# Optimization experiments

Hardware: AMD Instinct MI355X
Metric: run time of the kernel (lower is better)

Reference implementation:

```python
import jax, jax.numpy as jnp
import numpy as np

B, S, D = 4, 2048, 1024
H = 8
HD = D // H            # 128 head dim
FF = 4096 // H         # 512 per-head expert hidden
E = 8                  # num experts
K = 2                  # top-k
MU, GAMMA = 0.7, 1.0
LN_EPS = 1e-5


def setup_inputs() -> dict:
    key = jax.random.key(0)
    ks = jax.random.split(key, 12)
    sc = lambda *shape: 1.0 / np.sqrt(shape[0])
    return {
        "x": jax.random.normal(ks[0], (B, S, D), jnp.float32),
        "momentum": jnp.zeros((B * S * H, HD), jnp.float32),
        # split proj (input_dim -> input_dim)
        "split_W": jax.random.normal(ks[1], (D, D), jnp.float32) * sc(D),
        "split_b": jnp.zeros((D,), jnp.float32),
        # gate (head_dim -> num_experts)
        "gate_W": jax.random.normal(ks[2], (HD, E), jnp.float32) * sc(HD),
        "gate_b": jnp.zeros((E,), jnp.float32),
        # stacked experts: Linear(HD->FF) ReLU Linear(FF->HD)
        "W1": jax.random.normal(ks[3], (E, HD, FF), jnp.float32) * sc(HD),
        "b1": jnp.zeros((E, FF), jnp.float32),
        "W2": jax.random.normal(ks[4], (E, FF, HD), jnp.float32) * sc(FF),
        "b2": jnp.zeros((E, HD), jnp.float32),
        # layernorm over head_dim
        "ln_g": jnp.ones((HD,), jnp.float32),
        "ln_b": jnp.zeros((HD,), jnp.float32),
        # merge proj
        "merge_W": jax.random.normal(ks[5], (D, D), jnp.float32) * sc(D),
        "merge_b": jnp.zeros((D,), jnp.float32),
    }


def _topk_gate(t, gate_W, gate_b):
    # t: [T, HD] -> dense gate weights [T, E] with only top-K nonzero
    logits = t @ gate_W + gate_b                       # [T, E]
    topv, topi = jax.lax.top_k(logits, K)              # [T, K]
    gates_k = jax.nn.softmax(topv, axis=-1)            # softmax over kept experts
    onehot = jax.nn.one_hot(topi, E, dtype=t.dtype)    # [T, K, E]
    return jnp.einsum("tk,tke->te", gates_k, onehot)   # scatter back


def reference(x, momentum, split_W, split_b, gate_W, gate_b,
              W1, b1, W2, b2, ln_g, ln_b, merge_W, merge_b):
    # split: [B,S,D] -> [B*S*H, HD]
    x_hat = x @ split_W + split_b
    t = x_hat.reshape(B * S * H, HD)

    gates = _topk_gate(t, gate_W, gate_b)              # [T, E]

    # all-experts dense compute (matches the source's per-expert loop)
    h = jax.nn.relu(jnp.einsum("td,edf->etf", t, W1) + b1[:, None, :])  # [E,T,FF]
    eo = jnp.einsum("etf,efd->etd", h, W2) + b2[:, None, :]             # [E,T,HD]
    expert_outputs = jnp.einsum("te,etd->td", gates, eo)                # [T,HD]

    new_momentum = -expert_outputs + MU * momentum
    out = t + GAMMA * new_momentum

    # layernorm over head_dim
    mean = out.mean(-1, keepdims=True)
    var = out.var(-1, keepdims=True)
    out = (out - mean) * jax.lax.rsqrt(var + LN_EPS) * ln_g + ln_b

    # merge: [T,HD] -> [B,S,D] -> linear
    o = out.reshape(B, S, D)
    final = o @ merge_W + merge_b
    return final, new_momentum
```

## Files before the change

kernel.cpp:

```cpp
#include <hip/hip_runtime.h>

#define NBATCH 4
#define NS 2048
#define ND 1024
#define NH 8
#define HD 128
#define NFF 512
#define NE 8
#define NT 65536
#define NBS 8192
#define MU_F 0.7f
#define LN_EPS_F 1e-5f
#define EPS_GATE 1e-4f

typedef __attribute__((ext_vector_type(4))) float f32x4;
typedef __attribute__((ext_vector_type(2))) double f64x2;
typedef __attribute__((ext_vector_type(8))) _Float16 f16x8;
typedef __attribute__((ext_vector_type(4))) _Float16 f16x4;
typedef __attribute__((ext_vector_type(2))) _Float16 f16x2;

__device__ __forceinline__ void gload_lds16(const void* g, void* l) {
  __builtin_amdgcn_global_load_lds(
      (const __attribute__((address_space(1))) unsigned int*)g,
      (__attribute__((address_space(3))) unsigned int*)l, 16, 0, 0);
}

__global__ void tr_cvt_all_kernel(const float* __restrict__ split_W, const float* __restrict__ merge_W,
                                  const float* __restrict__ W1, const float* __restrict__ W2,
                                  _Float16* __restrict__ sWt, _Float16* __restrict__ mWt,
                                  _Float16* __restrict__ W1t, _Float16* __restrict__ W2t) {
  __shared__ float tile[32][33];
  int id = blockIdx.x;
  const float* in; _Float16* out; int R, C, bx, by, b;
  if (id < 1024)      { in = split_W; out = sWt; R = ND;  C = ND;  bx = id & 31; by = id >> 5; b = 0; }
  else if (id < 2048) { id -= 1024; in = merge_W; out = mWt; R = ND;  C = ND;  bx = id & 31; by = id >> 5; b = 0; }
  else if (id < 2560) { id -= 2048; in = W1; out = W1t; R = HD;  C = NFF; bx = id & 15; by = (id >> 4) & 3; b = id >> 6; }
  else                { id -= 2560; in = W2; out = W2t; R = NFF; C = HD;  bx = id & 3;  by = (id >> 2) & 15; b = id >> 6; }
  const float* inp = in + (size_t)b * R * C;
  _Float16* outp = out + (size_t)b * R * C;
  int c = bx * 32 + threadIdx.x;
  int r0 = by * 32;
  #pragma unroll
  for (int i = 0; i < 4; i++) {
    int r = r0 + threadIdx.y + i * 8;
    tile[threadIdx.y + i * 8][threadIdx.x] = inp[(size_t)r * C + c];
  }
  __syncthreads();
  int rr = r0 + threadIdx.x;
  #pragma unroll
  for (int i = 0; i < 4; i++) {
    int cc = bx * 32 + threadIdx.y + i * 8;
    outp[(size_t)cc * R + rr] = (_Float16)tile[threadIdx.x][threadIdx.y + i * 8];
  }
}

__global__ void build_G_kernel(const float* __restrict__ split_W, const float* __restrict__ split_b,
                               const float* __restrict__ gate_W, const float* __restrict__ gate_b,
                               double* __restrict__ G, float* __restrict__ Gq,
                               double* __restrict__ gbias, int* __restrict__ cnt) {
  int idx = blockIdx.x * 256 + threadIdx.x;
  if (blockIdx.x == 0 && threadIdx.x < 256) { cnt[threadIdx.x] = 0; cnt[threadIdx.x + 256] = 0; }
  int d = idx >> 6, o = idx & 63, h = o >> 3, e = o & 7;
  double acc = 0.0;
  const float* r0 = split_W + (size_t)d * ND + h * 128;
  #pragma unroll 4
  for (int j = 0; j < 128; j++)
    acc += (double)r0[j] * (double)gate_W[j * 8 + e];
  G[((size_t)(d >> 1) * 64 + o) * 2 + (d & 1)] = acc;
  Gq[((size_t)(d >> 2) * 64 + o) * 4 + (d & 3)] = (float)acc;
  if (idx < 64) {
    double bacc = 0.0;
    for (int j = 0; j < 128; j++)
      bacc += (double)split_b[h * 128 + j] * (double)gate_W[j * 8 + e];
    gbias[idx] = bacc + (double)gate_b[e];
  }
}

__global__ __launch_bounds__(256) void gate_kernel(const float* __restrict__ x,
    const float* __restrict__ Gq, const f64x2* __restrict__ Gx2, const double* __restrict__ gbias,
    _Float16* __restrict__ x_h,
    float* __restrict__ tkw, int* __restrict__ lists, int* __restrict__ cnt) {
  __shared__ float Gsq[16 * 256];
  __shared__ float xsf[16 * 68];
  __shared__ float lg[16 * 64];
  __shared__ int lcnt[8];
  __shared__ int lbase[8];
  int tid = threadIdx.x, lane = tid & 63, w = tid >> 6;
  int bs0 = blockIdx.x * 16;
  float accA[4], accB[4];
  #pragma unroll
  for (int r = 0; r < 4; r++) { accA[r] = 0.f; accB[r] = 0.f; }
  int xrow = tid >> 4, xc4 = tid & 15;
  const float* xr = xsf + (w * 4) * 68;
  if (tid < 8) lcnt[tid] = 0;

  for (int ch = 0; ch < 16; ch++) {
    __syncthreads();
    float4 xv4 = *(const float4*)(x + (size_t)(bs0 + xrow) * ND + ch * 64 + xc4 * 4);
    *(float4*)&xsf[xrow * 68 + xc4 * 4] = xv4;
    f16x4 xh = { (_Float16)xv4.x, (_Float16)xv4.y, (_Float16)xv4.z, (_Float16)xv4.w };
    *(f16x4*)(x_h + (size_t)(bs0 + xrow) * ND + ch * 64 + xc4 * 4) = xh;
    #pragma unroll
    for (int j = 0; j < 4; j++) {
      int n = j * 256 + tid;
      gload_lds16(Gq + (size_t)ch * 4096 + n * 4, Gsq + n * 4);
    }
    __syncthreads();
    #pragma unroll 4
    for (int kq = 0; kq < 16; kq++) {
      float4 g = *(const float4*)&Gsq[kq * 256 + lane * 4];
      #pragma unroll
      for (int r = 0; r < 4; r++) {
        float4 xv = *(const float4*)(xr + r * 68 + kq * 4);
        accA[r] = fmaf(xv.x, g.x, accA[r]);
        accB[r] = fmaf(xv.y, g.y, accB[r]);
        accA[r] = fmaf(xv.z, g.z, accA[r]);
        accB[r] = fmaf(xv.w, g.w, accB[r]);
      }
    }
  }
  float gbf = (float)gbias[lane];
  #pragma unroll
  for (int r = 0; r < 4; r++)
    lg[(w * 4 + r) * 64 + lane] = accA[r] + accB[r] + gbf;
  __syncthreads();

  int i1 = 0, i2 = 0, token = 0, p1 = 0, p2 = 0;
  if (tid < 128) {
    int row = tid >> 3, h = tid & 7;
    const float* L = lg + row * 64 + h * 8;
    float v1 = L[0];
    #pragma unroll
    for (int e2 = 1; e2 < 8; e2++) if (L[e2] > v1) { v1 = L[e2]; i1 = e2; }
    i2 = -1; float v2 = -1e30f;
    #pragma unroll
    for (int e2 = 0; e2 < 8; e2++) if (e2 != i1 && L[e2] > v2) { v2 = L[e2]; i2 = e2; }
    float v3 = -1e30f;
    #pragma unroll
    for (int e2 = 0; e2 < 8; e2++) if (e2 != i1 && e2 != i2 && L[e2] > v3) v3 = L[e2];
    float g1 = 0.f, g2 = 0.f;
    bool amb = !((v1 - v2 >= EPS_GATE) && (v2 - v3 >= EPS_GATE));
    if (!amb) {
      float ex = expf(v2 - v1);
      float den = 1.f + ex;
      g1 = 1.f / den; g2 = ex / den;
    }
    unsigned long long mask = __ballot(amb);
    while (mask) {
      int src = __ffsll((long long)mask) - 1;
      mask &= mask - 1;
      int srow = __shfl(row, src, 64);
      int sh   = __shfl(h, src, 64);
      double part[8];
      #pragma unroll
      for (int e2 = 0; e2 < 8; e2++) part[e2] = 0.0;
      const float* xg = x + (size_t)(bs0 + srow) * ND + lane * 16;
      #pragma unroll
      for (int kk = 0; kk < 8; kk++) {
        double x0 = (double)xg[kk * 2], x1 = (double)xg[kk * 2 + 1];
        const f64x2* gp = Gx2 + (size_t)(lane * 8 + kk) * 64 + sh * 8;
        #pragma unroll
        for (int e2 = 0; e2 < 8; e2++) {
          f64x2 g = gp[e2];
          part[e2] += x0 * g.x + x1 * g.y;
        }
      }
      #pragma unroll
      for (int m = 1; m < 64; m <<= 1)
        #pragma unroll
        for (int e2 = 0; e2 < 8; e2++) part[e2] += __shfl_xor(part[e2], m, 64);
      if (lane == src) {
        double L64[8];
        #pragma unroll
        for (int e2 = 0; e2 < 8; e2++) L64[e2] = part[e2] + gbias[sh * 8 + e2];
        i1 = 0; double d1 = L64[0];
        #pragma unroll
        for (int e2 = 1; e2 < 8; e2++) if (L64[e2] > d1) { d1 = L64[e2]; i1 = e2; }
        i2 = -1; double d2 = -1e300;
        #pragma unroll
        for (int e2 = 0; e2 < 8; e2++) if (e2 != i1 && L64[e2] > d2) { d2 = L64[e2]; i2 = e2; }
        float ex = expf((float)(d2 - d1));
        float den = 1.f + ex;
        g1 = 1.f / den; g2 = ex / den;
      }
    }
    token = (bs0 + row) * 8 + h;
    tkw[token * 2]     = g1;
    tkw[token * 2 + 1] = g2;
    p1 = atomicAdd(&lcnt[i1], 1);
    p2 = atomicAdd(&lcnt[i2], 1);
  }
  __syncthreads();
  if (tid < 8) lbase[tid] = atomicAdd(cnt + tid * 64, lcnt[tid]);
  __syncthreads();
  if (tid < 128) {
    lists[(size_t)i1 * NT + lbase[i1] + p1] = token * 2;
    lists[(size_t)i2 * NT + lbase[i2] + p2] = token * 2 + 1;
  }
}

__global__ __launch_bounds__(256) void gemm_f16_kernel(
    const _Float16* __restrict__ A, const _Float16* __restrict__ Bt,
    const float* __restrict__ bias, float* __restrict__ Cf, _Float16* __restrict__ Ch,
    int M, int N, int Kd) {
  __shared__ _Float16 As[128 * 32];
  __shared__ _Float16 Bs[128 * 32];
  int tid = threadIdx.x, lane = tid & 63, w = tid >> 6;
  int wr = w >> 1, wc = w & 1;
  int lid = blockIdx.y * 8 + blockIdx.x;
  int xcd = lid & 7, sub = (lid >> 3) & 7, grp = lid >> 6;
  int m0 = (xcd * 8 + sub) * 128;
  int n0 = grp * 128;
  f32x4 acc[4][4];
  #pragma unroll
  for (int i = 0; i < 4; i++)
    #pragma unroll
    for (int j = 0; j < 4; j++) acc[i][j] = (f32x4){0.f, 0.f, 0.f, 0.f};
  int srow = lane >> 2, scol = (lane & 3) * 8;
  int fr = lane & 15, ko = (lane >> 4) * 8;
  const _Float16* Ag = A + (size_t)(m0 + srow) * Kd + scol;
  const _Float16* Bg = Bt + (size_t)(n0 + srow) * Kd + scol;

  for (int k0 = 0; k0 < Kd; k0 += 32) {
    #pragma unroll
    for (int j = 0; j < 2; j++) {
      int rb = (w * 2 + j) * 16;
      gload_lds16(Ag + (size_t)rb * Kd + k0, As + rb * 32);
      gload_lds16(Bg + (size_t)rb * Kd + k0, Bs + rb * 32);
    }
    __syncthreads();
    f16x8 af[4], bq[4];
    #pragma unroll
    for (int mi = 0; mi < 4; mi++) af[mi] = *(const f16x8*)(As + (wr * 64 + mi * 16 + fr) * 32 + ko);
    #pragma unroll
    for (int ni = 0; ni < 4; ni++) bq[ni] = *(const f16x8*)(Bs + (wc * 64 + ni * 16 + fr) * 32 + ko);
    __syncthreads();
    #pragma unroll
    for (int mi = 0; mi < 4; mi++)
      #pragma unroll
      for (int ni = 0; ni < 4; ni++)
        acc[mi][ni] = __builtin_amdgcn_mfma_f32_16x16x32_f16(af[mi], bq[ni], acc[mi][ni], 0, 0, 0);
  }
  int rbase = m0 + wr * 64 + ((lane >> 4) << 2);
  int cbase = n0 + wc * 64 + (lane & 15);
  #pragma unroll
  for (int mi = 0; mi < 4; mi++)
    #pragma unroll
    for (int ni = 0; ni < 4; ni++) {
      int cc = cbase + ni * 16;
      float bv = bias ? bias[cc] : 0.f;
      #pragma unroll
      for (int r = 0; r < 4; r++) {
        int rr = rbase + mi * 16 + r;
        float v = acc[mi][ni][r] + bv;
        if (Cf) Cf[(size_t)rr * N + cc] = v;
        if (Ch) Ch[(size_t)rr * N + cc] = (_Float16)v;
      }
    }
}

__global__ __launch_bounds__(512, 2) void expert_kernel(
    const _Float16* __restrict__ t_h, const _Float16* __restrict__ W1t, const _Float16* __restrict__ W2t,
    const float* __restrict__ b1, const float* __restrict__ b2,
    const int* __restrict__ cnt, const int* __restrict__ lists, const float* __restrict__ tkw,
    _Float16* __restrict__ slots) {
  int e = blockIdx.x & 7;
  int m0 = (blockIdx.x >> 3) * 128;
  int count = cnt[e * 64];
  if (m0 >= count) return;
  __shared__ _Float16 ring[3][64 * 128];
  __shared__ _Float16 h_s[128 * 64];
  __shared__ float b1s[NFF];
  __shared__ float b2s[HD];
  __shared__ int alist[128];
  __shared__ float aw[128];
  int tid = threadIdx.x, lane = tid & 63, w = tid >> 6;
  int wr = w >> 1, wc = w & 1;
  int fr = lane & 15, g = lane >> 4;

  if (tid < 128) {
    int idx = m0 + tid;
    int a = (idx < count) ? lists[(size_t)e * NT + idx] : -1;
    alist[tid] = a;
    aw[tid] = (a >= 0) ? tkw[a] : 0.f;
  }
  b1s[tid] = b1[e * NFF + tid];
  if (tid < 128) b2s[tid] = b2[e * HD + tid];
  __syncthreads();

  auto stage = [&](int p) {
    if (p >= 16) return;
    int ch = p >> 1;
    _Float16* dst = &ring[p % 3][0];
    if ((p & 1) == 0) {
      #pragma unroll
      for (int j = 0; j < 2; j++) {
        int n = j * 512 + tid;
        int r = n >> 4, gg = n & 15;
        int sg = gg ^ ((r >> 1) & 7);
        gload_lds16(W1t + (size_t)e * (NFF * HD) + (size_t)(ch * 64 + r) * HD + sg * 8, dst + n * 8);
      }
    } else {
      #pragma unroll
      for (int j = 0; j < 2; j++) {
        int n = j * 512 + tid;
        int r = n >> 3, gg = n & 7;
        int sg = gg ^ ((r >> 1) & 7);
        gload_lds16(W2t + (size_t)e * (HD * NFF) + (size_t)r * NFF + ch * 64 + sg * 8, dst + n * 8);
      }
    }
  };

  f16x8 af[2][4];
  #pragma unroll
  for (int mi = 0; mi < 2; mi++) {
    int rloc = wr * 32 + mi * 16 + fr;
    int a = alist[rloc];
    const _Float16* tb = t_h + (size_t)(a >> 1) * HD;
    #pragma unroll
    for (int ks = 0; ks < 4; ks++) {
      f16x8 v = {0, 0, 0, 0, 0, 0, 0, 0};
      if (a >= 0) v = *(const f16x8*)(tb + ks * 32 + g * 8);
      af[mi][ks] = v;
    }
  }
  asm volatile("s_waitcnt vmcnt(0)" ::: "memory");
  stage(0); stage(1);
  asm volatile("s_waitcnt vmcnt(2) lgkmcnt(0)\n\ts_barrier" ::: "memory");

  f32x4 acc2[2][4];
  #pragma unroll
  for (int i = 0; i < 2; i++)
    #pragma unroll
    for (int j = 0; j < 4; j++) acc2[i][j] = (f32x4){0.f, 0.f, 0.f, 0.f};

  #pragma unroll
  for (int p = 0; p < 16; p++) {
    stage(p + 2);
    int ch = p >> 1;
    const char* WB = (const char*)&ring[p % 3][0];
    if ((p & 1) == 0) {
      float b1r[2][4];
      #pragma unroll
      for (int ni = 0; ni < 2; ni++)
        #pragma unroll
        for (int r = 0; r < 4; r++)
          b1r[ni][r] = b1s[ch * 64 + wc * 32 + ni * 16 + g * 4 + r];
      f32x4 acc1[2][2];
      #pragma unroll
      for (int i = 0; i < 2; i++)
        #pragma unroll
        for (int j = 0; j < 2; j++) acc1[i][j] = (f32x4){0.f, 0.f, 0.f, 0.f};
      #pragma unroll
      for (int ks = 0; ks < 4; ks++) {
        f16x8 bq[2];
        #pragma unroll
        for (int ni = 0; ni < 2; ni++) {
          int rw = wc * 32 + ni * 16 + fr;
          int byte = rw * 256 + ((ks * 64 + g * 16) ^ (((rw >> 1) & 7) << 4));
          bq[ni] = *(const f16x8*)(WB + byte);
        }
        #pragma unroll
        for (int mi = 0; mi < 2; mi++)
          #pragma unroll
          for (int ni = 0; ni < 2; ni++)
            acc1[mi][ni] = __builtin_amdgcn_mfma_f32_16x16x32_f16(bq[ni], af[mi][ks], acc1[mi][ni], 0, 0, 0);
      }
      #pragma unroll
      for (int mi = 0; mi < 2; mi++)
        #pragma unroll
        for (int ni = 0; ni < 2; ni++) {
          f16x4 hv;
          #pragma unroll
          for (int r = 0; r < 4; r++)
            hv[r] = (_Float16)fmaxf(acc1[mi][ni][r] + b1r[ni][r], 0.f);
          int tok = wr * 32 + mi * 16 + fr;
          int foff = wc * 64 + ni * 32 + g * 8;
          int byte = tok * 128 + (foff ^ (((tok >> 1) & 7) << 4));
          *(f16x4*)((char*)h_s + byte) = hv;
        }
    } else {
      #pragma unroll
      for (int ks = 0; ks < 2; ks++) {
        f16x8 ah[2], bq[4];
        #pragma unroll
        for (int mi = 0; mi < 2; mi++) {
          int row = wr * 32 + mi * 16 + fr;
          int byte = row * 128 + ((ks * 64 + g * 16) ^ (((row >> 1) & 7) << 4));
          ah[mi] = *(const f16x8*)((const char*)h_s + byte);
        }
        #pragma unroll
        for (int ni = 0; ni < 4; ni++) {
          int rw = wc * 64 + ni * 16 + fr;
          int byte = rw * 128 + ((ks * 64 + g * 16) ^ (((rw >> 1) & 7) << 4));
          bq[ni] = *(const f16x8*)((const char*)&ring[p % 3][0] + byte);
        }
        #pragma unroll
        for (int mi = 0; mi < 2; mi++)
          #pragma unroll
          for (int ni = 0; ni < 4; ni++)
            acc2[mi][ni] = __builtin_amdgcn_mfma_f32_16x16x32_f16(ah[mi], bq[ni], acc2[mi][ni], 0, 0, 0);
      }
    }
    if (p == 14) {
      asm volatile("s_waitcnt vmcnt(0) lgkmcnt(0)\n\ts_barrier" ::: "memory");
    } else if (p < 14) {
      asm volatile("s_waitcnt vmcnt(2) lgkmcnt(0)\n\ts_barrier" ::: "memory");
    }
  }
  #pragma unroll
  for (int mi = 0; mi < 2; mi++)
    #pragma unroll
    for (int ni = 0; ni < 4; ni++) {
      int ncol = wc * 64 + ni * 16 + fr;
      float bv = b2s[ncol];
      #pragma unroll
      for (int r = 0; r < 4; r++) {
        int m = wr * 32 + mi * 16 + g * 4 + r;
        int a = alist[m];
        if (a >= 0)
          slots[(size_t)a * HD + ncol] = (_Float16)(aw[m] * (acc2[mi][ni][r] + bv));
      }
    }
}

__global__ __launch_bounds__(256) void combine_ln_kernel(
    const _Float16* __restrict__ slots, const float* __restrict__ momentum,
    const _Float16* __restrict__ t_h, const float* __restrict__ ln_g, const float* __restrict__ ln_b,
    float* __restrict__ nm_out, _Float16* __restrict__ out_h) {
  int w = threadIdx.x >> 6, lane = threadIdx.x & 63;
  int tok = blockIdx.x * 4 + w;
  int d0 = lane * 2;
  f16x2 s0 = *(const f16x2*)(slots + (size_t)tok * 256 + d0);
  f16x2 s1 = *(const f16x2*)(slots + (size_t)tok * 256 + 128 + d0);
  float2 mo = *(const float2*)(momentum + (size_t)tok * HD + d0);
  f16x2 tv = *(const f16x2*)(t_h + (size_t)tok * HD + d0);
  float nm0 = -((float)s0.x + (float)s1.x) + MU_F * mo.x;
  float nm1 = -((float)s0.y + (float)s1.y) + MU_F * mo.y;
  float2 nm2; nm2.x = nm0; nm2.y = nm1;
  *(float2*)(nm_out + (size_t)tok * HD + d0) = nm2;
  float r0 = (float)tv.x + nm0;
  float r1 = (float)tv.y + nm1;
  float s = r0 + r1, sq = r0 * r0 + r1 * r1;
  #pragma unroll
  for (int m = 1; m < 64; m <<= 1) { s += __shfl_xor(s, m, 64); sq += __shfl_xor(sq, m, 64); }
  float mean = s * (1.f / 128.f);
  float var = sq * (1.f / 128.f) - mean * mean;
  float is = rsqrtf(var + LN_EPS_F);
  float y0 = (r0 - mean) * is * ln_g[d0] + ln_b[d0];
  float y1 = (r1 - mean) * is * ln_g[d0 + 1] + ln_b[d0 + 1];
  f16x2 yo = { (_Float16)y0, (_Float16)y1 };
  *(f16x2*)(out_h + (size_t)tok * HD + d0) = yo;
}

extern "C" void kernel_launch(void* const* d_in, const int* in_sizes, int n_in,
                              void* d_out, int out_size, void* d_ws, size_t ws_size,
                              hipStream_t stream) {
  const float* x        = (const float*)d_in[0];
  const float* momentum = (const float*)d_in[1];
  const float* split_W  = (const float*)d_in[2];
  const float* split_b  = (const float*)d_in[3];
  const float* gate_W   = (const float*)d_in[4];
  const float* gate_b   = (const float*)d_in[5];
  const float* W1       = (const float*)d_in[6];
  const float* b1       = (const float*)d_in[7];
  const float* W2       = (const float*)d_in[8];
  const float* b2       = (const float*)d_in[9];
  const float* ln_g     = (const float*)d_in[10];
  const float* ln_b     = (const float*)d_in[11];
  const float* merge_W  = (const float*)d_in[12];
  const float* merge_b  = (const float*)d_in[13];
  float* final_out = (float*)d_out;
  float* nm_out    = final_out + (size_t)NBS * ND;

  char* ws = (char*)d_ws;
  size_t off = 0;
  auto alloc = [&](size_t bytes) { void* p = ws + off; off = (off + bytes + 255) & ~(size_t)255; return p; };
  _Float16* x_h   = (_Float16*)alloc((size_t)NBS * ND * 2);
  _Float16* t_h   = (_Float16*)alloc((size_t)NT * HD * 2);
  _Float16* out_h = (_Float16*)alloc((size_t)NT * HD * 2);
  _Float16* sWt   = (_Float16*)alloc((size_t)ND * ND * 2);
  _Float16* mWt   = (_Float16*)alloc((size_t)ND * ND * 2);
  _Float16* W1t   = (_Float16*)alloc((size_t)NE * HD * NFF * 2);
  _Float16* W2t   = (_Float16*)alloc((size_t)NE * HD * NFF * 2);
  f64x2*    Gx2   = (f64x2*)alloc((size_t)512 * 64 * 16);
  float*    Gq    = (float*)alloc((size_t)512 * 64 * 8);
  double*   gbias = (double*)alloc(64 * 8);
  float*    tkw   = (float*)alloc((size_t)NT * 2 * 4);
  int*      lists = (int*)alloc((size_t)NE * NT * 4);
  int*      cnt   = (int*)alloc(512 * 4);
  _Float16* slots = (_Float16*)alloc((size_t)NT * 2 * HD * 2);
  (void)in_sizes; (void)n_in; (void)out_size; (void)ws_size;

  tr_cvt_all_kernel<<<3072, dim3(32, 8), 0, stream>>>(split_W, merge_W, W1, W2, sWt, mWt, W1t, W2t);
  build_G_kernel<<<256, 256, 0, stream>>>(split_W, split_b, gate_W, gate_b, (double*)Gx2, Gq, gbias, cnt);
  gate_kernel<<<512, 256, 0, stream>>>(x, Gq, Gx2, gbias, x_h, tkw, lists, cnt);
  gemm_f16_kernel<<<dim3(8, 64), 256, 0, stream>>>(x_h, sWt, split_b, nullptr, t_h, NBS, ND, ND);
  expert_kernel<<<NE * 512, 512, 0, stream>>>(t_h, W1t, W2t, b1, b2, cnt, lists, tkw, slots);
  combine_ln_kernel<<<NT / 4, 256, 0, stream>>>(slots, momentum, t_h, ln_g, ln_b, nm_out, out_h);
  gemm_f16_kernel<<<dim3(8, 64), 256, 0, stream>>>(out_h, mWt, merge_b, final_out, nullptr, NBS, ND, ND);
}
```

Baseline: 220.3 us.

## Fuse prep kernels and widen GEMM K-tile to 64 with XOR-swizzled LDS

Merges the weight transpose/convert kernel and the gate-matrix build kernel into one launch, removing a kernel launch boundary. The f16 GEMM used for the split and merge projections now loads 64-wide K tiles per barrier pair instead of 32, which halves the number of sync points. It stores the LDS tiles with an XOR swizzle to avoid bank conflicts on the fragment reads. LDS use per block doubles, which may reduce occupancy.

```diff
diff --git a/kernel.cpp b/kernel.cpp
--- a/kernel.cpp
+++ b/kernel.cpp
@@ -25,12 +25,36 @@
       (__attribute__((address_space(3))) unsigned int*)l, 16, 0, 0);
 }
 
-__global__ void tr_cvt_all_kernel(const float* __restrict__ split_W, const float* __restrict__ merge_W,
-                                  const float* __restrict__ W1, const float* __restrict__ W2,
-                                  _Float16* __restrict__ sWt, _Float16* __restrict__ mWt,
-                                  _Float16* __restrict__ W1t, _Float16* __restrict__ W2t) {
+__global__ void prep_kernel(const float* __restrict__ split_W, const float* __restrict__ merge_W,
+                            const float* __restrict__ W1, const float* __restrict__ W2,
+                            const float* __restrict__ split_b, const float* __restrict__ gate_W,
+                            const float* __restrict__ gate_b,
+                            _Float16* __restrict__ sWt, _Float16* __restrict__ mWt,
+                            _Float16* __restrict__ W1t, _Float16* __restrict__ W2t,
+                            double* __restrict__ G, float* __restrict__ Gq,
+                            double* __restrict__ gbias, int* __restrict__ cnt) {
+  int id = blockIdx.x;
+  if (id >= 3072) {
+    int tid = threadIdx.y * 32 + threadIdx.x;
+    int idx = (id - 3072) * 256 + tid;
+    if (id == 3072) { cnt[tid] = 0; cnt[tid + 256] = 0; }
+    int d = idx >> 6, o = idx & 63, h = o >> 3, e = o & 7;
+    double acc = 0.0;
+    const float* r0 = split_W + (size_t)d * ND + h * 128;
+    #pragma unroll 4
+    for (int j = 0; j < 128; j++)
+      acc += (double)r0[j] * (double)gate_W[j * 8 + e];
+    G[((size_t)(d >> 1) * 64 + o) * 2 + (d & 1)] = acc;
+    Gq[((size_t)(d >> 2) * 64 + o) * 4 + (d & 3)] = (float)acc;
+    if (idx < 64) {
+      double bacc = 0.0;
+      for (int j = 0; j < 128; j++)
+        bacc += (double)split_b[h * 128 + j] * (double)gate_W[j * 8 + e];
+      gbias[idx] = bacc + (double)gate_b[e];
+    }
+    return;
+  }
   __shared__ float tile[32][33];
-  int id = blockIdx.x;
   const float* in; _Float16* out; int R, C, bx, by, b;
   if (id < 1024)      { in = split_W; out = sWt; R = ND;  C = ND;  bx = id & 31; by = id >> 5; b = 0; }
   else if (id < 2048) { id -= 1024; in = merge_W; out = mWt; R = ND;  C = ND;  bx = id & 31; by = id >> 5; b = 0; }
@@ -51,28 +75,6 @@
   for (int i = 0; i < 4; i++) {
     int cc = bx * 32 + threadIdx.y + i * 8;
     outp[(size_t)cc * R + rr] = (_Float16)tile[threadIdx.x][threadIdx.y + i * 8];
-  }
-}
-
-__global__ void build_G_kernel(const float* __restrict__ split_W, const float* __restrict__ split_b,
-                               const float* __restrict__ gate_W, const float* __restrict__ gate_b,
-                               double* __restrict__ G, float* __restrict__ Gq,
-                               double* __restrict__ gbias, int* __restrict__ cnt) {
-  int idx = blockIdx.x * 256 + threadIdx.x;
-  if (blockIdx.x == 0 && threadIdx.x < 256) { cnt[threadIdx.x] = 0; cnt[threadIdx.x + 256] = 0; }
-  int d = idx >> 6, o = idx & 63, h = o >> 3, e = o & 7;
-  double acc = 0.0;
-  const float* r0 = split_W + (size_t)d * ND + h * 128;
-  #pragma unroll 4
-  for (int j = 0; j < 128; j++)
-    acc += (double)r0[j] * (double)gate_W[j * 8 + e];
-  G[((size_t)(d >> 1) * 64 + o) * 2 + (d & 1)] = acc;
-  Gq[((size_t)(d >> 2) * 64 + o) * 4 + (d & 3)] = (float)acc;
-  if (idx < 64) {
-    double bacc = 0.0;
-    for (int j = 0; j < 128; j++)
-      bacc += (double)split_b[h * 128 + j] * (double)gate_W[j * 8 + e];
-    gbias[idx] = bacc + (double)gate_b[e];
   }
 }
 
@@ -203,8 +205,8 @@
     const _Float16* __restrict__ A, const _Float16* __restrict__ Bt,
     const float* __restrict__ bias, float* __restrict__ Cf, _Float16* __restrict__ Ch,
     int M, int N, int Kd) {
-  __shared__ _Float16 As[128 * 32];
-  __shared__ _Float16 Bs[128 * 32];
+  __shared__ _Float16 As[128 * 64];
+  __shared__ _Float16 Bs[128 * 64];
   int tid = threadIdx.x, lane = tid & 63, w = tid >> 6;
   int wr = w >> 1, wc = w & 1;
   int lid = blockIdx.y * 8 + blockIdx.x;
@@ -216,30 +218,40 @@
   for (int i = 0; i < 4; i++)
     #pragma unroll
     for (int j = 0; j < 4; j++) acc[i][j] = (f32x4){0.f, 0.f, 0.f, 0.f};
-  int srow = lane >> 2, scol = (lane & 3) * 8;
-  int fr = lane & 15, ko = (lane >> 4) * 8;
-  const _Float16* Ag = A + (size_t)(m0 + srow) * Kd + scol;
-  const _Float16* Bg = Bt + (size_t)(n0 + srow) * Kd + scol;
-
-  for (int k0 = 0; k0 < Kd; k0 += 32) {
-    #pragma unroll
-    for (int j = 0; j < 2; j++) {
-      int rb = (w * 2 + j) * 16;
-      gload_lds16(Ag + (size_t)rb * Kd + k0, As + rb * 32);
-      gload_lds16(Bg + (size_t)rb * Kd + k0, Bs + rb * 32);
+  int fr = lane & 15, ko = lane >> 4;
+
+  for (int k0 = 0; k0 < Kd; k0 += 64) {
+    #pragma unroll
+    for (int j = 0; j < 4; j++) {
+      int n = j * 256 + tid;
+      int r = n >> 3, gg = n & 7;
+      int sg = gg ^ ((r >> 1) & 7);
+      gload_lds16(A + (size_t)(m0 + r) * Kd + k0 + sg * 8, As + n * 8);
+      gload_lds16(Bt + (size_t)(n0 + r) * Kd + k0 + sg * 8, Bs + n * 8);
     }
     __syncthreads();
-    f16x8 af[4], bq[4];
-    #pragma unroll
-    for (int mi = 0; mi < 4; mi++) af[mi] = *(const f16x8*)(As + (wr * 64 + mi * 16 + fr) * 32 + ko);
-    #pragma unroll
-    for (int ni = 0; ni < 4; ni++) bq[ni] = *(const f16x8*)(Bs + (wc * 64 + ni * 16 + fr) * 32 + ko);
+    #pragma unroll
+    for (int kh = 0; kh < 2; kh++) {
+      f16x8 af[4], bq[4];
+      #pragma unroll
+      for (int mi = 0; mi < 4; mi++) {
+        int row = wr * 64 + mi * 16 + fr;
+        int byte = row * 128 + ((kh * 64 + ko * 16) ^ (((row >> 1) & 7) << 4));
+        af[mi] = *(const f16x8*)((const char*)As + byte);
+      }
+      #pragma unroll
+      for (int ni = 0; ni < 4; ni++) {
+        int row = wc * 64 + ni * 16 + fr;
+        int byte = row * 128 + ((kh * 64 + ko * 16) ^ (((row >> 1) & 7) << 4));
+        bq[ni] = *(const f16x8*)((const char*)Bs + byte);
+      }
+      #pragma unroll
+      for (int mi = 0; mi < 4; mi++)
+        #pragma unroll
+        for (int ni = 0; ni < 4; ni++)
+          acc[mi][ni] = __builtin_amdgcn_mfma_f32_16x16x32_f16(af[mi], bq[ni], acc[mi][ni], 0, 0, 0);
+    }
     __syncthreads();
-    #pragma unroll
-    for (int mi = 0; mi < 4; mi++)
-      #pragma unroll
-      for (int ni = 0; ni < 4; ni++)
-        acc[mi][ni] = __builtin_amdgcn_mfma_f32_16x16x32_f16(af[mi], bq[ni], acc[mi][ni], 0, 0, 0);
   }
   int rbase = m0 + wr * 64 + ((lane >> 4) << 2);
   int cbase = n0 + wc * 64 + (lane & 15);
@@ -492,8 +504,8 @@
   _Float16* slots = (_Float16*)alloc((size_t)NT * 2 * HD * 2);
   (void)in_sizes; (void)n_in; (void)out_size; (void)ws_size;
 
-  tr_cvt_all_kernel<<<3072, dim3(32, 8), 0, stream>>>(split_W, merge_W, W1, W2, sWt, mWt, W1t, W2t);
-  build_G_kernel<<<256, 256, 0, stream>>>(split_W, split_b, gate_W, gate_b, (double*)Gx2, Gq, gbias, cnt);
+  prep_kernel<<<3328, dim3(32, 8), 0, stream>>>(split_W, merge_W, W1, W2, split_b, gate_W, gate_b,
+                                                sWt, mWt, W1t, W2t, (double*)Gx2, Gq, gbias, cnt);
   gate_kernel<<<512, 256, 0, stream>>>(x, Gq, Gx2, gbias, x_h, tkw, lists, cnt);
   gemm_f16_kernel<<<dim3(8, 64), 256, 0, stream>>>(x_h, sWt, split_b, nullptr, t_h, NBS, ND, ND);
   expert_kernel<<<NE * 512, 512, 0, stream>>>(t_h, W1t, W2t, b1, b2, cnt, lists, tkw, slots);
```

Result: faster. 208.0 us (median of 2 runs) (-5.6%).
